# Kernel tuning notes

Hardware: AMD Instinct MI355X
Metric: run time of the kernel (lower is better)

The kernel has to match this reference:

```python
import jax, jax.numpy as jnp
import numpy as np

DIM = 64
N_EMBED = 512
COMMITMENT_COST = 0.25


def setup_inputs() -> dict:
    key = jax.random.key(0)
    k1, k2 = jax.random.split(key)
    z = jax.random.normal(k1, (64, 32, 32, DIM), dtype=jnp.float32)
    # nn.Embedding weight initialized uniform(-1/n_embed, 1/n_embed)
    embed_w = jax.random.uniform(
        k2, (N_EMBED, DIM), dtype=jnp.float32,
        minval=-1.0 / N_EMBED, maxval=1.0 / N_EMBED)
    return {"z": z, "embed_w": embed_w}


def reference(z, embed_w):
    # z: [B, H, W, D] -> flatten to [N, D]
    z_flat = z.reshape(-1, z.shape[-1])
    # squared L2 distances via ||a||^2 + ||b||^2 - 2 a.b : [N, n_embed]
    distances = (
        jnp.sum(z_flat ** 2, axis=1, keepdims=True)
        + jnp.sum(embed_w ** 2, axis=1)
        - 2.0 * jnp.matmul(z_flat, embed_w.T)
    )
    min_encoding_indices = jnp.argmin(distances, axis=1)[:, None]  # [N, 1]
    z_q = embed_w[min_encoding_indices].reshape(z.shape)  # gather + reshape
    commitment_loss = COMMITMENT_COST * jnp.mean(
        (z - jax.lax.stop_gradient(z_q)) ** 2)
    return (z_q, min_encoding_indices, commitment_loss)
```

## Files before the change

### kernel.cpp

```cpp
#include <hip/hip_runtime.h>

#define NROWS 65536
#define DIM   64
#define NE    512

#define WS_PRESPLIT 0
#define WS_PREY     131072
#define WS_YNORM    139264
#define WS_ACC      141312
#define WS_TICKET   141320

typedef __attribute__((ext_vector_type(8)))  short bf16x8;
typedef __attribute__((ext_vector_type(16))) float f32x16;

static __device__ __forceinline__ unsigned short bf16rne(float x) {
    unsigned int u = __float_as_uint(x);
    u += 0x7FFFu + ((u >> 16) & 1u);
    return (unsigned short)(u >> 16);
}
static __device__ __forceinline__ float bf16tof(unsigned short h) {
    return __uint_as_float(((unsigned int)h) << 16);
}

__global__ __launch_bounds__(256) void vq_prep(
    const float* __restrict__ ew, char* ws)
{
    const int r = blockIdx.x * 256 + threadIdx.x;
    if (r == 0) {
        *(unsigned long long*)(ws + WS_ACC)    = 0ull;
        *(unsigned long long*)(ws + WS_TICKET) = 0ull;
    }
    float a[64];
    const float4* src = (const float4*)(ew + (size_t)r * DIM);
    #pragma unroll
    for (int q = 0; q < 16; ++q) {
        float4 v = src[q];
        a[q*4+0]=v.x; a[q*4+1]=v.y; a[q*4+2]=v.z; a[q*4+3]=v.w;
    }
    float rc[8];
    #pragma unroll
    for (int j = 0; j < 8; ++j) rc[j] = __fmul_rn(a[j], a[j]);
    #pragma unroll
    for (int i = 8; i < 64; i += 8)
        #pragma unroll
        for (int j = 0; j < 8; ++j)
            rc[j] = __fadd_rn(rc[j], __fmul_rn(a[i+j], a[i+j]));
    float Y = __fadd_rn(__fadd_rn(__fadd_rn(rc[0],rc[1]),__fadd_rn(rc[2],rc[3])),
                        __fadd_rn(__fadd_rn(rc[4],rc[5]),__fadd_rn(rc[6],rc[7])));
    ((float*)(ws + WS_YNORM))[r] = Y;
    unsigned short ynh = bf16rne(Y);
    unsigned short ynl = bf16rne(Y - bf16tof(ynh));
    bf16x8 py = {};
    py[0] = (short)ynh; py[1] = (short)ynl;
    *(bf16x8*)(ws + WS_PREY + r*16) = py;
    const int sw = (r & 7) << 4;
    char* base = ws + WS_PRESPLIT + (size_t)r * 256;
    #pragma unroll
    for (int c = 0; c < 8; ++c) {
        bf16x8 h, l;
        #pragma unroll
        for (int j = 0; j < 8; ++j) {
            float x = -2.0f * a[c*8+j];
            unsigned short hb = bf16rne(x);
            h[j] = (short)hb;
            l[j] = (short)bf16rne(x - bf16tof(hb));
        }
        int off = (c*16) ^ sw;
        *(bf16x8*)(base + off)       = h;
        *(bf16x8*)(base + off + 128) = l;
    }
}

__global__ __launch_bounds__(1024) void vq_fused(
    const float* __restrict__ z, const float* __restrict__ ew,
    char* ws, float* out)
{
    __shared__ __align__(16) char ldsA[131072];
    __shared__ __align__(16) char ldsY[8192];
    __shared__ float4 mrg[8][32];
    __shared__ int    rwin[256];
    __shared__ float  rdist[256];
    __shared__ float  rX[256];
    __shared__ float  zs[64];
    __shared__ float  rd8[8];
    __shared__ int    ri8[8];
    __shared__ unsigned int flagbits[8];
    __shared__ float  wred[4];

    const int tid  = threadIdx.x;
    const int lane = tid & 63;
    const int wv   = tid >> 6;
    const int rg   = wv >> 1;
    const int eh   = wv & 1;
    const int hh   = lane >> 5;
    const int l31  = lane & 31;
    const int R0   = blockIdx.x * 256;
    const int zrow = R0 + rg*32 + l31;
    const int eoff = eh * 256;

    if (tid < 8) flagbits[tid] = 0u;

    bf16x8 zh[4], zl[4];
    float xacc = 0.f;
    {
        const float* zp = z + (size_t)zrow * DIM + hh * 8;
        #pragma unroll
        for (int kt = 0; kt < 4; ++kt) {
            float4 p0 = *(const float4*)(zp + kt*16);
            float4 p1 = *(const float4*)(zp + kt*16 + 4);
            float a[8] = {p0.x,p0.y,p0.z,p0.w,p1.x,p1.y,p1.z,p1.w};
            bf16x8 hv, lv;
            #pragma unroll
            for (int j = 0; j < 8; ++j) {
                unsigned short hb = bf16rne(a[j]);
                hv[j] = (short)hb;
                lv[j] = (short)bf16rne(a[j] - bf16tof(hb));
                xacc  = fmaf(a[j], a[j], xacc);
            }
            zh[kt] = hv; zl[kt] = lv;
        }
    }

    #pragma unroll 1
    for (int i = 0; i < 9; ++i) {
        int idx = tid + 1024 * i;
        if (idx < 8704) {
            float4 v = *(const float4*)(ws + idx*16);
            if (idx < 8192) *(float4*)(ldsA + idx*16) = v;
            else            *(float4*)(ldsY + (idx - 8192)*16) = v;
        }
    }
    __syncthreads();

    const bf16x8 zero8 = {};
    bf16x8 bones = {};
    if (hh == 0) { bones[0] = (short)0x3F80; bones[1] = (short)0x3F80; }

    float d1 = 3.4e38f, d2 = 3.4e38f;
    int   i1 = 0;

    #pragma unroll 1
    for (int t = 0; t < 8; ++t) {
        const int   e0    = eoff + t*32;
        const int   arow  = e0 + l31;
        const char* abase = ldsA + arow*256;
        const int   sw    = (arow & 7) << 4;

        f32x16 acc;
        #pragma unroll
        for (int g = 0; g < 16; ++g) acc[g] = 0.f;

        bf16x8 ay = zero8;
        if (hh == 0) ay = *(const bf16x8*)(ldsY + arow*16);
        acc = __builtin_amdgcn_mfma_f32_32x32x16_bf16(ay, bones, acc, 0,0,0);

        #pragma unroll
        for (int kt = 0; kt < 4; ++kt) {
            const int kb = (kt*32 + hh*16) ^ sw;
            bf16x8 ah = *(const bf16x8*)(abase + kb);
            bf16x8 al = *(const bf16x8*)(abase + kb + 128);
            acc = __builtin_amdgcn_mfma_f32_32x32x16_bf16(ah, zh[kt], acc, 0,0,0);
            acc = __builtin_amdgcn_mfma_f32_32x32x16_bf16(ah, zl[kt], acc, 0,0,0);
            acc = __builtin_amdgcn_mfma_f32_32x32x16_bf16(al, zh[kt], acc, 0,0,0);
        }

        const int ebase = e0 + 4*hh;
        #pragma unroll
        for (int g = 0; g < 16; ++g) {
            float d = acc[g];
            int   e = ebase + (g & 3) + 8*(g >> 2);
            d2 = fminf(fmaxf(d, d1), d2);
            bool bt = d < d1;
            i1 = bt ? e : i1;
            d1 = fminf(d, d1);
        }
    }

    float od1 = __shfl_xor(d1, 32, 64);
    int   oi1 = __shfl_xor(i1, 32, 64);
    float od2 = __shfl_xor(d2, 32, 64);
    bool  oth = (od1 < d1) || (od1 == d1 && oi1 < i1);
    int   wiw = oth ? oi1 : i1;
    float s1w = fminf(d1, od1);
    float s2w = fminf(fmaxf(d1, od1), fminf(d2, od2));
    float X   = xacc + __shfl_xor(xacc, 32, 64);

    if (eh == 1 && hh == 0)
        mrg[rg][l31] = make_float4(s1w, __int_as_float(wiw), s2w, 0.f);
    __syncthreads();
    if (eh == 0 && hh == 0) {
        float4 b = mrg[rg][l31];
        float s1b = b.x, s2b = b.z;
        int   ib  = __float_as_int(b.y);
        bool  tA  = (s1w <= s1b);
        int   wi  = tA ? wiw : ib;
        float s1  = fminf(s1w, s1b);
        float s2  = fminf(fmaxf(s1w, s1b), fminf(s2w, s2b));
        float Xs  = X + 1e-3f;
        float ue  = __uint_as_float(__float_as_uint(Xs) & 0x7F800000u) * 1.1920929e-7f;
        bool  flag = (s2 - s1) < (2.0f * ue + 2e-6f);
        int r = rg*32 + l31;
        rwin[r]  = wi;
        rdist[r] = s1;
        rX[r]    = X;
        if (flag) atomicOr(&flagbits[rg], 1u << l31);
    }
    __syncthreads();

    const float* yn = (const float*)(ws + WS_YNORM);
    for (int g8 = 0; g8 < 8; ++g8) {
        unsigned bits = flagbits[g8];
        while (bits) {
            int r = g8*32 + __ffs(bits) - 1;
            bits &= bits - 1;
            if (tid < 16)
                *(float4*)(zs + tid*4) =
                    *(const float4*)(z + (size_t)(R0 + r) * DIM + tid*4);
            __syncthreads();
            float rc[8];
            #pragma unroll
            for (int j = 0; j < 8; ++j) rc[j] = __fmul_rn(zs[j], zs[j]);
            #pragma unroll
            for (int i = 8; i < 64; i += 8)
                #pragma unroll
                for (int j = 0; j < 8; ++j)
                    rc[j] = __fadd_rn(rc[j], __fmul_rn(zs[i+j], zs[i+j]));
            float xn = __fadd_rn(__fadd_rn(__fadd_rn(rc[0],rc[1]),__fadd_rn(rc[2],rc[3])),
                                 __fadd_rn(__fadd_rn(rc[4],rc[5]),__fadd_rn(rc[6],rc[7])));
            float bd = 3.4e38f; int bi = NE;
            if (tid < NE) {
                const int e = tid;
                const float* ep = ew + (size_t)e * DIM;
                double m0 = 0.0, m1 = 0.0, m2 = 0.0, m3 = 0.0;
                #pragma unroll
                for (int q = 0; q < 16; ++q) {
                    float4 ev = *(const float4*)(ep + q*4);
                    m0 = fma((double)zs[q*4+0], (double)ev.x, m0);
                    m1 = fma((double)zs[q*4+1], (double)ev.y, m1);
                    m2 = fma((double)zs[q*4+2], (double)ev.z, m2);
                    m3 = fma((double)zs[q*4+3], (double)ev.w, m3);
                }
                double m = (m0 + m1) + (m2 + m3);
                float W = __fadd_rn(xn, yn[e]);
                float d = __fadd_rn(W, -(2.0f * (float)m));
                bd = d; bi = e;
            }
            #pragma unroll
            for (int off = 32; off >= 1; off >>= 1) {
                float od = __shfl_xor(bd, off, 64);
                int   oi = __shfl_xor(bi, off, 64);
                if (od < bd || (od == bd && oi < bi)) { bd = od; bi = oi; }
            }
            if (lane == 0 && wv < 8) { rd8[wv] = bd; ri8[wv] = bi; }
            __syncthreads();
            if (tid == 0) {
                float fd = rd8[0]; int fi = ri8[0];
                #pragma unroll
                for (int k = 1; k < 8; ++k)
                    if (rd8[k] < fd || (rd8[k] == fd && ri8[k] < fi)) { fd = rd8[k]; fi = ri8[k]; }
                rwin[r]  = fi;
                rdist[r] = fd;
                rX[r]    = 0.f;
            }
            __syncthreads();
        }
    }

    if (tid < 256)
        out[(size_t)NROWS*DIM + R0 + tid] = (float)rwin[tid];

    #pragma unroll
    for (int i = 0; i < 4; ++i) {
        int f4  = tid + 1024 * i;
        int row = f4 >> 4;
        int c4  = f4 & 15;
        float4 v = *(const float4*)(ew + (size_t)rwin[row] * DIM + c4 * 4);
        *(float4*)(out + (size_t)R0 * DIM + (size_t)f4 * 4) = v;
    }

    float term = (tid < 256) ? (rX[tid] + rdist[tid]) : 0.f;
    #pragma unroll
    for (int off = 32; off >= 1; off >>= 1) term += __shfl_xor(term, off, 64);
    if (lane == 0 && wv < 4) wred[wv] = term;
    __syncthreads();
    if (tid == 0) {
        float part = wred[0] + wred[1] + wred[2] + wred[3];
        unsigned long long q =
            (unsigned long long)((double)part * 268435456.0 + 0.5);
        atomicAdd((unsigned long long*)(ws + WS_ACC), q);
        __threadfence();
        unsigned int tk = atomicAdd((unsigned int*)(ws + WS_TICKET), 1u);
        if (tk == 255u) {
            unsigned long long tot =
                atomicAdd((unsigned long long*)(ws + WS_ACC), 0ull);
            out[(size_t)NROWS*DIM + NROWS] =
                (float)(0.25 * ((double)tot / 268435456.0)
                        / (double)((size_t)NROWS * DIM));
        }
    }
}

extern "C" void kernel_launch(void* const* d_in, const int* in_sizes, int n_in,
                              void* d_out, int out_size, void* d_ws, size_t ws_size,
                              hipStream_t stream) {
    const float* z  = (const float*)d_in[0];
    const float* ew = (const float*)d_in[1];
    float* out = (float*)d_out;
    char*  ws  = (char*)d_ws;
    vq_prep <<<2,   256,  0, stream>>>(ew, ws);
    vq_fused<<<256, 1024, 0, stream>>>(z, ew, ws, out);
}
```

Before: 53.79 us.

## Tile each wave over 64 rows x 128 codes and planarize codebook layout

Each wave now computes distances for two 32-row tiles against a quarter of the codebook, instead of one 32-row tile against half of it. Each codebook fragment read from LDS is reused for two MFMA row tiles, halving LDS reads per MFMA. The prep kernel writes the split bf16 codebook as k-planes (plane x 512 rows x 16 bytes) instead of swizzled 256-byte rows, so lane reads are contiguous. The cross-wave argmin merge now combines four partial results per row. The trade-off is higher VGPR use from doubled z fragments and accumulators.

Result: slower. 68.94 us (+28.1%).

```diff
diff --git a/kernel.cpp b/kernel.cpp
--- a/kernel.cpp
+++ b/kernel.cpp
@@ -53,8 +53,6 @@
     bf16x8 py = {};
     py[0] = (short)ynh; py[1] = (short)ynl;
     *(bf16x8*)(ws + WS_PREY + r*16) = py;
-    const int sw = (r & 7) << 4;
-    char* base = ws + WS_PRESPLIT + (size_t)r * 256;
     #pragma unroll
     for (int c = 0; c < 8; ++c) {
         bf16x8 h, l;
@@ -65,9 +63,10 @@
             h[j] = (short)hb;
             l[j] = (short)bf16rne(x - bf16tof(hb));
         }
-        int off = (c*16) ^ sw;
-        *(bf16x8*)(base + off)       = h;
-        *(bf16x8*)(base + off + 128) = l;
+        int kt = c >> 1, hhp = c & 1;
+        int plane = kt*4 + hhp*2;
+        *(bf16x8*)(ws + WS_PRESPLIT + (size_t)plane*8192 + r*16)       = h;
+        *(bf16x8*)(ws + WS_PRESPLIT + (size_t)(plane+1)*8192 + r*16)   = l;
     }
 }
 
@@ -77,7 +76,7 @@
 {
     __shared__ __align__(16) char ldsA[131072];
     __shared__ __align__(16) char ldsY[8192];
-    __shared__ float4 mrg[8][32];
+    __shared__ float4 mrg[4][256];
     __shared__ int    rwin[256];
     __shared__ float  rdist[256];
     __shared__ float  rX[256];
@@ -90,34 +89,42 @@
     const int tid  = threadIdx.x;
     const int lane = tid & 63;
     const int wv   = tid >> 6;
-    const int rg   = wv >> 1;
-    const int eh   = wv & 1;
+    const int rg   = wv >> 2;
+    const int eh   = wv & 3;
     const int hh   = lane >> 5;
     const int l31  = lane & 31;
     const int R0   = blockIdx.x * 256;
-    const int zrow = R0 + rg*32 + l31;
-    const int eoff = eh * 256;
+    const int eoff = eh * 128;
 
     if (tid < 8) flagbits[tid] = 0u;
 
-    bf16x8 zh[4], zl[4];
-    float xacc = 0.f;
+    bf16x8 zh0[4], zl0[4], zh1[4], zl1[4];
+    float xacc_a = 0.f, xacc_b = 0.f;
     {
-        const float* zp = z + (size_t)zrow * DIM + hh * 8;
+        const float* zpA = z + (size_t)(R0 + rg*64 + l31) * DIM + hh * 8;
+        const float* zpB = zpA + 32 * DIM;
         #pragma unroll
         for (int kt = 0; kt < 4; ++kt) {
-            float4 p0 = *(const float4*)(zp + kt*16);
-            float4 p1 = *(const float4*)(zp + kt*16 + 4);
-            float a[8] = {p0.x,p0.y,p0.z,p0.w,p1.x,p1.y,p1.z,p1.w};
-            bf16x8 hv, lv;
+            float4 p0 = *(const float4*)(zpA + kt*16);
+            float4 p1 = *(const float4*)(zpA + kt*16 + 4);
+            float4 q0 = *(const float4*)(zpB + kt*16);
+            float4 q1 = *(const float4*)(zpB + kt*16 + 4);
+            float aA[8] = {p0.x,p0.y,p0.z,p0.w,p1.x,p1.y,p1.z,p1.w};
+            float aB[8] = {q0.x,q0.y,q0.z,q0.w,q1.x,q1.y,q1.z,q1.w};
+            bf16x8 hA, lA, hB, lB;
             #pragma unroll
             for (int j = 0; j < 8; ++j) {
-                unsigned short hb = bf16rne(a[j]);
-                hv[j] = (short)hb;
-                lv[j] = (short)bf16rne(a[j] - bf16tof(hb));
-                xacc  = fmaf(a[j], a[j], xacc);
-            }
-            zh[kt] = hv; zl[kt] = lv;
+                unsigned short hb = bf16rne(aA[j]);
+                hA[j] = (short)hb;
+                lA[j] = (short)bf16rne(aA[j] - bf16tof(hb));
+                xacc_a = fmaf(aA[j], aA[j], xacc_a);
+                unsigned short hc = bf16rne(aB[j]);
+                hB[j] = (short)hc;
+                lB[j] = (short)bf16rne(aB[j] - bf16tof(hc));
+                xacc_b = fmaf(aB[j], aB[j], xacc_b);
+            }
+            zh0[kt] = hA; zl0[kt] = lA;
+            zh1[kt] = hB; zl1[kt] = lB;
         }
     }
 
@@ -136,74 +143,97 @@
     bf16x8 bones = {};
     if (hh == 0) { bones[0] = (short)0x3F80; bones[1] = (short)0x3F80; }
 
-    float d1 = 3.4e38f, d2 = 3.4e38f;
-    int   i1 = 0;
+    float d1a = 3.4e38f, d2a = 3.4e38f, d1b = 3.4e38f, d2b = 3.4e38f;
+    int   i1a = 0, i1b = 0;
 
     #pragma unroll 1
-    for (int t = 0; t < 8; ++t) {
-        const int   e0    = eoff + t*32;
-        const int   arow  = e0 + l31;
-        const char* abase = ldsA + arow*256;
-        const int   sw    = (arow & 7) << 4;
-
-        f32x16 acc;
-        #pragma unroll
-        for (int g = 0; g < 16; ++g) acc[g] = 0.f;
+    for (int t = 0; t < 4; ++t) {
+        const int e0   = eoff + t*32;
+        const int arow = e0 + l31;
+
+        f32x16 acc0, acc1;
+        #pragma unroll
+        for (int g = 0; g < 16; ++g) { acc0[g] = 0.f; acc1[g] = 0.f; }
 
         bf16x8 ay = zero8;
         if (hh == 0) ay = *(const bf16x8*)(ldsY + arow*16);
-        acc = __builtin_amdgcn_mfma_f32_32x32x16_bf16(ay, bones, acc, 0,0,0);
+        acc0 = __builtin_amdgcn_mfma_f32_32x32x16_bf16(ay, bones, acc0, 0,0,0);
+        acc1 = __builtin_amdgcn_mfma_f32_32x32x16_bf16(ay, bones, acc1, 0,0,0);
 
         #pragma unroll
         for (int kt = 0; kt < 4; ++kt) {
-            const int kb = (kt*32 + hh*16) ^ sw;
-            bf16x8 ah = *(const bf16x8*)(abase + kb);
-            bf16x8 al = *(const bf16x8*)(abase + kb + 128);
-            acc = __builtin_amdgcn_mfma_f32_32x32x16_bf16(ah, zh[kt], acc, 0,0,0);
-            acc = __builtin_amdgcn_mfma_f32_32x32x16_bf16(ah, zl[kt], acc, 0,0,0);
-            acc = __builtin_amdgcn_mfma_f32_32x32x16_bf16(al, zh[kt], acc, 0,0,0);
+            const char* pb = ldsA + (size_t)(kt*4 + hh*2)*8192 + arow*16;
+            bf16x8 ah = *(const bf16x8*)(pb);
+            bf16x8 al = *(const bf16x8*)(pb + 8192);
+            acc0 = __builtin_amdgcn_mfma_f32_32x32x16_bf16(ah, zh0[kt], acc0, 0,0,0);
+            acc1 = __builtin_amdgcn_mfma_f32_32x32x16_bf16(ah, zh1[kt], acc1, 0,0,0);
+            acc0 = __builtin_amdgcn_mfma_f32_32x32x16_bf16(ah, zl0[kt], acc0, 0,0,0);
+            acc1 = __builtin_amdgcn_mfma_f32_32x32x16_bf16(ah, zl1[kt], acc1, 0,0,0);
+            acc0 = __builtin_amdgcn_mfma_f32_32x32x16_bf16(al, zh0[kt], acc0, 0,0,0);
+            acc1 = __builtin_amdgcn_mfma_f32_32x32x16_bf16(al, zh1[kt], acc1, 0,0,0);
         }
 
         const int ebase = e0 + 4*hh;
         #pragma unroll
         for (int g = 0; g < 16; ++g) {
-            float d = acc[g];
-            int   e = ebase + (g & 3) + 8*(g >> 2);
-            d2 = fminf(fmaxf(d, d1), d2);
-            bool bt = d < d1;
-            i1 = bt ? e : i1;
-            d1 = fminf(d, d1);
-        }
-    }
-
-    float od1 = __shfl_xor(d1, 32, 64);
-    int   oi1 = __shfl_xor(i1, 32, 64);
-    float od2 = __shfl_xor(d2, 32, 64);
-    bool  oth = (od1 < d1) || (od1 == d1 && oi1 < i1);
-    int   wiw = oth ? oi1 : i1;
-    float s1w = fminf(d1, od1);
-    float s2w = fminf(fmaxf(d1, od1), fminf(d2, od2));
-    float X   = xacc + __shfl_xor(xacc, 32, 64);
-
-    if (eh == 1 && hh == 0)
-        mrg[rg][l31] = make_float4(s1w, __int_as_float(wiw), s2w, 0.f);
+            int e = ebase + (g & 3) + 8*(g >> 2);
+            float da = acc0[g], db = acc1[g];
+            d2a = fminf(fmaxf(da, d1a), d2a);
+            bool ba = da < d1a; i1a = ba ? e : i1a; d1a = fminf(da, d1a);
+            d2b = fminf(fmaxf(db, d1b), d2b);
+            bool bb = db < d1b; i1b = bb ? e : i1b; d1b = fminf(db, d1b);
+        }
+    }
+
+    float s1a, s2a, s1b, s2b, Xa, Xb;
+    int   wia, wib;
+    {
+        float od1 = __shfl_xor(d1a, 32, 64);
+        int   oi1 = __shfl_xor(i1a, 32, 64);
+        float od2 = __shfl_xor(d2a, 32, 64);
+        bool  oth = (od1 < d1a) || (od1 == d1a && oi1 < i1a);
+        wia = oth ? oi1 : i1a;
+        s1a = fminf(d1a, od1);
+        s2a = fminf(fmaxf(d1a, od1), fminf(d2a, od2));
+        Xa  = xacc_a + __shfl_xor(xacc_a, 32, 64);
+    }
+    {
+        float od1 = __shfl_xor(d1b, 32, 64);
+        int   oi1 = __shfl_xor(i1b, 32, 64);
+        float od2 = __shfl_xor(d2b, 32, 64);
+        bool  oth = (od1 < d1b) || (od1 == d1b && oi1 < i1b);
+        wib = oth ? oi1 : i1b;
+        s1b = fminf(d1b, od1);
+        s2b = fminf(fmaxf(d1b, od1), fminf(d2b, od2));
+        Xb  = xacc_b + __shfl_xor(xacc_b, 32, 64);
+    }
+
+    if (hh == 0) {
+        mrg[eh][rg*64 + l31]      = make_float4(s1a, __int_as_float(wia), s2a, 0.f);
+        mrg[eh][rg*64 + 32 + l31] = make_float4(s1b, __int_as_float(wib), s2b, 0.f);
+    }
     __syncthreads();
     if (eh == 0 && hh == 0) {
-        float4 b = mrg[rg][l31];
-        float s1b = b.x, s2b = b.z;
-        int   ib  = __float_as_int(b.y);
-        bool  tA  = (s1w <= s1b);
-        int   wi  = tA ? wiw : ib;
-        float s1  = fminf(s1w, s1b);
-        float s2  = fminf(fmaxf(s1w, s1b), fminf(s2w, s2b));
-        float Xs  = X + 1e-3f;
-        float ue  = __uint_as_float(__float_as_uint(Xs) & 0x7F800000u) * 1.1920929e-7f;
-        bool  flag = (s2 - s1) < (2.0f * ue + 2e-6f);
-        int r = rg*32 + l31;
-        rwin[r]  = wi;
-        rdist[r] = s1;
-        rX[r]    = X;
-        if (flag) atomicOr(&flagbits[rg], 1u << l31);
+        #pragma unroll
+        for (int s = 0; s < 2; ++s) {
+            int   r = rg*64 + s*32 + l31;
+            float X = s ? Xb : Xa;
+            float s1 = 3.4e38f, s2 = 3.4e38f;
+            int   i1 = 0;
+            #pragma unroll
+            for (int q = 0; q < 4; ++q) {
+                float4 v = mrg[q][r];
+                if (v.x < s1) { s2 = fminf(s1, v.z); s1 = v.x; i1 = __float_as_int(v.y); }
+                else          { s2 = fminf(s2, v.x); }
+            }
+            float Xs = X + 1e-3f;
+            float ue = __uint_as_float(__float_as_uint(Xs) & 0x7F800000u) * 1.1920929e-7f;
+            bool  flag = (s2 - s1) < (2.0f * ue + 2e-6f);
+            rwin[r]  = i1;
+            rdist[r] = s1;
+            rX[r]    = X;
+            if (flag) atomicOr(&flagbits[r >> 5], 1u << (r & 31));
+        }
     }
     __syncthreads();
 
```

## Pack distance and index into sortable unsigned keys and use planar codebook layout

Applied to the files above, without the earlier changes.

Distances are offset by 2, scaled to fixed point, and packed with the code index in the low 9 bits so top-two tracking becomes unsigned min/max trees instead of float compare-and-select chains. The codebook split layout changes from swizzled per-row to planar per-k-slice arrays, making LDS reads contiguous per lane without XOR addressing. The quantised keys lose precision, so the near-tie margin is widened to send more rows to the exact fallback path. It assumes distances stay within the fixed-point range.

New measurement: 63.59 us. 1.18x slower.

```diff
diff --git a/kernel.cpp b/kernel.cpp
--- a/kernel.cpp
+++ b/kernel.cpp
@@ -21,6 +21,8 @@
 static __device__ __forceinline__ float bf16tof(unsigned short h) {
     return __uint_as_float(((unsigned int)h) << 16);
 }
+static __device__ __forceinline__ unsigned umn(unsigned a, unsigned b) { return a < b ? a : b; }
+static __device__ __forceinline__ unsigned umx(unsigned a, unsigned b) { return a > b ? a : b; }
 
 __global__ __launch_bounds__(256) void vq_prep(
     const float* __restrict__ ew, char* ws)
@@ -53,8 +55,6 @@
     bf16x8 py = {};
     py[0] = (short)ynh; py[1] = (short)ynl;
     *(bf16x8*)(ws + WS_PREY + r*16) = py;
-    const int sw = (r & 7) << 4;
-    char* base = ws + WS_PRESPLIT + (size_t)r * 256;
     #pragma unroll
     for (int c = 0; c < 8; ++c) {
         bf16x8 h, l;
@@ -65,9 +65,10 @@
             h[j] = (short)hb;
             l[j] = (short)bf16rne(x - bf16tof(hb));
         }
-        int off = (c*16) ^ sw;
-        *(bf16x8*)(base + off)       = h;
-        *(bf16x8*)(base + off + 128) = l;
+        int kt = c >> 1, hhp = c & 1;
+        int plane = kt*4 + hhp*2;
+        *(bf16x8*)(ws + WS_PRESPLIT + (size_t)plane*8192 + r*16)       = h;
+        *(bf16x8*)(ws + WS_PRESPLIT + (size_t)(plane+1)*8192 + r*16)   = l;
     }
 }
 
@@ -77,7 +78,7 @@
 {
     __shared__ __align__(16) char ldsA[131072];
     __shared__ __align__(16) char ldsY[8192];
-    __shared__ float4 mrg[8][32];
+    __shared__ uint2  mrg[256];
     __shared__ int    rwin[256];
     __shared__ float  rdist[256];
     __shared__ float  rX[256];
@@ -136,19 +137,16 @@
     bf16x8 bones = {};
     if (hh == 0) { bones[0] = (short)0x3F80; bones[1] = (short)0x3F80; }
 
-    float d1 = 3.4e38f, d2 = 3.4e38f;
-    int   i1 = 0;
+    unsigned M1 = 0xFFFFFFFFu, M2 = 0xFFFFFFFFu;
 
     #pragma unroll 1
     for (int t = 0; t < 8; ++t) {
-        const int   e0    = eoff + t*32;
-        const int   arow  = e0 + l31;
-        const char* abase = ldsA + arow*256;
-        const int   sw    = (arow & 7) << 4;
+        const int e0   = eoff + t*32;
+        const int arow = e0 + l31;
 
         f32x16 acc;
         #pragma unroll
-        for (int g = 0; g < 16; ++g) acc[g] = 0.f;
+        for (int g = 0; g < 16; ++g) acc[g] = 2.0f;
 
         bf16x8 ay = zero8;
         if (hh == 0) ay = *(const bf16x8*)(ldsY + arow*16);
@@ -156,54 +154,70 @@
 
         #pragma unroll
         for (int kt = 0; kt < 4; ++kt) {
-            const int kb = (kt*32 + hh*16) ^ sw;
-            bf16x8 ah = *(const bf16x8*)(abase + kb);
-            bf16x8 al = *(const bf16x8*)(abase + kb + 128);
+            const char* pb = ldsA + (size_t)(kt*4 + hh*2)*8192 + arow*16;
+            bf16x8 ah = *(const bf16x8*)(pb);
+            bf16x8 al = *(const bf16x8*)(pb + 8192);
             acc = __builtin_amdgcn_mfma_f32_32x32x16_bf16(ah, zh[kt], acc, 0,0,0);
             acc = __builtin_amdgcn_mfma_f32_32x32x16_bf16(ah, zl[kt], acc, 0,0,0);
             acc = __builtin_amdgcn_mfma_f32_32x32x16_bf16(al, zh[kt], acc, 0,0,0);
         }
 
         const int ebase = e0 + 4*hh;
+        unsigned en[16];
         #pragma unroll
         for (int g = 0; g < 16; ++g) {
-            float d = acc[g];
-            int   e = ebase + (g & 3) + 8*(g >> 2);
-            d2 = fminf(fmaxf(d, d1), d2);
-            bool bt = d < d1;
-            i1 = bt ? e : i1;
-            d1 = fminf(d, d1);
-        }
-    }
-
-    float od1 = __shfl_xor(d1, 32, 64);
-    int   oi1 = __shfl_xor(i1, 32, 64);
-    float od2 = __shfl_xor(d2, 32, 64);
-    bool  oth = (od1 < d1) || (od1 == d1 && oi1 < i1);
-    int   wiw = oth ? oi1 : i1;
-    float s1w = fminf(d1, od1);
-    float s2w = fminf(fmaxf(d1, od1), fminf(d2, od2));
-    float X   = xacc + __shfl_xor(xacc, 32, 64);
-
-    if (eh == 1 && hh == 0)
-        mrg[rg][l31] = make_float4(s1w, __int_as_float(wiw), s2w, 0.f);
+            unsigned e = (unsigned)(ebase + (g & 3) + 8*(g >> 2));
+            unsigned u = (unsigned)(acc[g] * 268435456.0f);
+            en[g] = (u & ~511u) | e;
+        }
+        unsigned pm[8], ps[8];
+        #pragma unroll
+        for (int p = 0; p < 8; ++p) {
+            pm[p] = umn(en[2*p], en[2*p+1]);
+            ps[p] = umx(en[2*p], en[2*p+1]);
+        }
+        #pragma unroll
+        for (int st = 4; st >= 1; st >>= 1)
+            #pragma unroll
+            for (int p = 0; p < 4; ++p) {
+                if (p < st) {
+                    unsigned hi = umx(pm[p], pm[p+st]);
+                    pm[p] = umn(pm[p], pm[p+st]);
+                    ps[p] = umn(umn(ps[p], ps[p+st]), hi);
+                }
+            }
+        unsigned hi0 = umx(M1, pm[0]);
+        M1 = umn(M1, pm[0]);
+        M2 = umn(M2, umn(hi0, ps[0]));
+    }
+
+    {
+        unsigned oM1 = (unsigned)__shfl_xor((int)M1, 32, 64);
+        unsigned oM2 = (unsigned)__shfl_xor((int)M2, 32, 64);
+        unsigned hi  = umx(M1, oM1);
+        M1 = umn(M1, oM1);
+        M2 = umn(umn(M2, oM2), hi);
+    }
+    float X = xacc + __shfl_xor(xacc, 32, 64);
+
+    if (eh == 1 && hh == 0) mrg[rg*32 + l31] = make_uint2(M1, M2);
     __syncthreads();
     if (eh == 0 && hh == 0) {
-        float4 b = mrg[rg][l31];
-        float s1b = b.x, s2b = b.z;
-        int   ib  = __float_as_int(b.y);
-        bool  tA  = (s1w <= s1b);
-        int   wi  = tA ? wiw : ib;
-        float s1  = fminf(s1w, s1b);
-        float s2  = fminf(fmaxf(s1w, s1b), fminf(s2w, s2b));
-        float Xs  = X + 1e-3f;
-        float ue  = __uint_as_float(__float_as_uint(Xs) & 0x7F800000u) * 1.1920929e-7f;
-        bool  flag = (s2 - s1) < (2.0f * ue + 2e-6f);
-        int r = rg*32 + l31;
-        rwin[r]  = wi;
+        uint2 o = mrg[rg*32 + l31];
+        unsigned hi = umx(M1, o.x);
+        M1 = umn(M1, o.x);
+        M2 = umn(umn(M2, o.y), hi);
+
+        int   r  = rg*32 + l31;
+        float s1 = (float)(M1 & ~511u) * 3.7252903e-09f - 2.0f;
+        float gap = (float)((M2 & ~511u) - (M1 & ~511u)) * 3.7252903e-09f;
+        float Xs = X + 1e-3f;
+        float ue = __uint_as_float(__float_as_uint(Xs) & 0x7F800000u) * 1.1920929e-7f;
+        bool  flag = gap < (2.0f * ue + 1.2e-5f);
+        rwin[r]  = (int)(M1 & 511u);
         rdist[r] = s1;
         rX[r]    = X;
-        if (flag) atomicOr(&flagbits[rg], 1u << l31);
+        if (flag) atomicOr(&flagbits[r >> 5], 1u << (r & 31));
     }
     __syncthreads();
 
```
